# Performance work log

Measured on AMD Instinct MI355X. Metric: run time of the kernel, lower is better.

The kernel has to match this reference:

```python
import jax, jax.numpy as jnp
import numpy as np

HEADS = 16
DIM_HEAD = 64
SCALE = float(np.sqrt(DIM_HEAD))  # NOTE: original code MULTIPLIES by sqrt(dim_head)


def setup_inputs() -> dict:
    key = jax.random.key(0)
    k1, k2, k3, k4 = jax.random.split(key, 4)
    dim = 1024
    b, n = 2, 2048
    s = 1.0 / np.sqrt(dim)
    return {
        "x": jax.random.normal(k1, (b, n, dim), dtype=jnp.float32),
        "w_q": jax.random.normal(k2, (dim, HEADS * DIM_HEAD), dtype=jnp.float32) * s,
        "w_vk": jax.random.normal(k3, (dim, HEADS * DIM_HEAD * 2), dtype=jnp.float32) * s,
        "w_out": jax.random.normal(k4, (HEADS * DIM_HEAD, dim), dtype=jnp.float32) * s,
    }


def reference(x, w_q, w_vk, w_out):
    b, n, _ = x.shape
    h, d = HEADS, DIM_HEAD
    context = x  # context=None, kv_include_self=False
    q = (x @ w_q).reshape(b, n, h, d).transpose(0, 2, 1, 3)          # b h n d
    kv = context @ w_vk                                              # b n 2hd
    k, v = jnp.split(kv, 2, axis=-1)                                 # chunk order: k first, v second
    k = k.reshape(b, n, h, d).transpose(0, 2, 1, 3)
    v = v.reshape(b, n, h, d).transpose(0, 2, 1, 3)
    dots = jnp.einsum('bhid,bhjd->bhij', q, k) * SCALE               # faithful: multiply by sqrt(d)
    attn = jax.nn.softmax(dots, axis=-1)                             # dropout p=0 -> identity
    out = jnp.einsum('bhij,bhjd->bhid', attn, v)
    out = out.transpose(0, 2, 1, 3).reshape(b, n, h * d)
    return out @ w_out
```

## Files before the change

kernel.cpp:

```cpp
#include <hip/hip_runtime.h>

typedef _Float16 half4 __attribute__((ext_vector_type(4)));
typedef _Float16 half8 __attribute__((ext_vector_type(8)));
typedef _Float16 h2pk __attribute__((ext_vector_type(2)));
typedef float f32x4 __attribute__((ext_vector_type(4)));

#define MFMA_F16K32(a, b, c) __builtin_amdgcn_mfma_f32_16x16x32_f16(a, b, c, 0, 0, 0)
#define MFMA_F16K16(a, b, c) __builtin_amdgcn_mfma_f32_16x16x16f16(a, b, c, 0, 0, 0)
#define EXP2F(x) __builtin_amdgcn_exp2f(x)
#define CVT_PK(a, b) __builtin_bit_cast(h2pk, __builtin_amdgcn_cvt_pkrtz(a, b))

constexpr int NSEQ = 2048, DIM = 1024;
constexpr float QSCALE = 11.5415603271f;

__device__ __forceinline__ void ld_lds16(void* lds, const void* g) {
  __builtin_amdgcn_global_load_lds(
      (const __attribute__((address_space(1))) void*)g,
      (__attribute__((address_space(3))) void*)lds, 16, 0, 0);
}

__global__ __launch_bounds__(256) void prep(
    const float* __restrict__ w_q, const float* __restrict__ w_vk,
    const float* __restrict__ w_out, const float* __restrict__ x,
    _Float16* __restrict__ WT, _Float16* __restrict__ WoT,
    _Float16* __restrict__ xf) {
  const int bid = blockIdx.x;
  const int t = threadIdx.x;
  if (bid >= 1024) {
    const size_t i = ((size_t)(bid - 1024) * 256 + t) * 8;
    float4 a = *(const float4*)(x + i), b2 = *(const float4*)(x + i + 4);
    float v[8] = {a.x, a.y, a.z, a.w, b2.x, b2.y, b2.z, b2.w};
    half8 h;
#pragma unroll
    for (int j = 0; j < 8; ++j) h[j] = (_Float16)v[j];
    *(half8*)(xf + i) = h;
    return;
  }
  __shared__ float T[64][65];
  const int bx = bid & 63, k0 = (bid >> 6) * 64;
  const float* src;
  int srcN, n0, dstrow, mode;
  float scale;
  if (bx < 16) {
    src = w_q; srcN = 1024; n0 = bx * 64; dstrow = n0; scale = QSCALE; mode = 0;
  } else if (bx < 48) {
    src = w_vk; srcN = 2048; n0 = (bx - 16) * 64; dstrow = 1024 + n0;
    scale = 1.0f; mode = 0;
  } else {
    src = w_out; srcN = 1024; n0 = (bx - 48) * 64; dstrow = n0;
    scale = 1.0f; mode = 1;
  }
  {
    const int r = t >> 2, c4 = (t & 3) * 16;
    const float* s = src + (size_t)(k0 + r) * srcN + n0 + c4;
    float4 v0 = ((const float4*)s)[0], v1 = ((const float4*)s)[1],
           v2 = ((const float4*)s)[2], v3 = ((const float4*)s)[3];
    *(float4*)&T[r][c4 + 0] = v0;  *(float4*)&T[r][c4 + 4] = v1;
    *(float4*)&T[r][c4 + 8] = v2;  *(float4*)&T[r][c4 + 12] = v3;
  }
  __syncthreads();
  const int rn = t >> 2, kc = (t & 3) * 16;
  half8 hv[2];
#pragma unroll
  for (int half = 0; half < 2; ++half)
#pragma unroll
    for (int j = 0; j < 8; ++j)
      hv[half][j] = (_Float16)(T[kc + half * 8 + j][rn] * scale);
  _Float16* d = ((mode == 0) ? WT + (size_t)(dstrow + rn) * 1024
                             : WoT + (size_t)(n0 + rn) * 1024) + k0 + kc;
  *(half8*)d = hv[0]; *(half8*)(d + 8) = hv[1];
}

__global__ __launch_bounds__(256, 3) void proj6(
    const _Float16* __restrict__ xf, const _Float16* __restrict__ WT,
    _Float16* __restrict__ qb, _Float16* __restrict__ kb,
    _Float16* __restrict__ VT) {
  __shared__ __align__(16) char smem[32768];
  const int t = threadIdx.x;
  const int lane = t & 63, wave = t >> 6, quad = lane >> 4, lq = lane & 15;
  const int bn = blockIdx.x * 128, bm = blockIdx.y * 128;
  const int kind = bn >> 10;
  const int wm = (wave >> 1) * 64, wn = (wave & 1) * 64;

  const int srow = lane >> 2;
  const int schk = (lane & 3) ^ (srow & 3);
  const _Float16* xg = xf + (size_t)(bm + wave * 32 + srow) * DIM + schk * 8;
  const _Float16* bg = WT + (size_t)(bn + wave * 32 + srow) * DIM + schk * 8;
  const int wb = wave * 2048;

  auto issue = [&](char* buf, int k0) {
    ld_lds16(buf + wb,                xg + k0);
    ld_lds16(buf + wb + 1024,         xg + k0 + 16 * DIM);
    ld_lds16(buf + 8192 + wb,         bg + k0);
    ld_lds16(buf + 8192 + wb + 1024,  bg + k0 + 16 * DIM);
  };

  const int swz = (quad ^ (lq & 3)) * 8;

  f32x4 acc[4][4];
#pragma unroll
  for (int i = 0; i < 4; ++i)
#pragma unroll
    for (int j = 0; j < 4; ++j) acc[i][j] = (f32x4){0.f, 0.f, 0.f, 0.f};

  char* bufA = smem;
  char* bufB = smem + 16384;
  issue(bufA, 0);
  for (int k0 = 0; k0 < DIM; k0 += 32) {
    char* cur = ((k0 >> 5) & 1) ? bufB : bufA;
    char* nxt = ((k0 >> 5) & 1) ? bufA : bufB;
    __syncthreads();
    if (k0 + 32 < DIM) issue(nxt, k0 + 32);
    const _Float16* Xs = (const _Float16*)cur;
    const _Float16* Bs = (const _Float16*)(cur + 8192);
    half8 ah[4];
#pragma unroll
    for (int i = 0; i < 4; ++i)
      ah[i] = *(const half8*)&Xs[(wm + i * 16 + lq) * 32 + swz];
#pragma unroll
    for (int j = 0; j < 4; ++j) {
      half8 bf = *(const half8*)&Bs[(wn + j * 16 + lq) * 32 + swz];
#pragma unroll
      for (int i = 0; i < 4; ++i) acc[i][j] = MFMA_F16K32(ah[i], bf, acc[i][j]);
    }
  }

  if (kind == 2) {
#pragma unroll
    for (int i = 0; i < 4; ++i)
#pragma unroll
      for (int j = 0; j < 4; ++j) {
        const int c = (bn - 2048) + wn + j * 16 + lq;
        const int row0 = bm + wm + i * 16 + quad * 4;
        const int b = row0 >> 11, n = row0 & 2047;
        const int h = c >> 6, d = c & 63;
        half4 o;
#pragma unroll
        for (int r = 0; r < 4; ++r) o[r] = (_Float16)acc[i][j][r];
        *(half4*)(VT + ((size_t)(b * 16 + h) * 64 + d) * 2048 + n) = o;
      }
  } else {
    _Float16* D = (kind == 0) ? qb : kb;
    const int cb = bn & 1023;
#pragma unroll
    for (int i = 0; i < 4; ++i)
#pragma unroll
      for (int j = 0; j < 4; ++j) {
        const int col = cb + wn + j * 16 + lq;
#pragma unroll
        for (int r = 0; r < 4; ++r) {
          const int row = bm + wm + i * 16 + quad * 4 + r;
          D[(size_t)row * 1024 + col] = (_Float16)acc[i][j][r];
        }
      }
  }
}

__global__ __launch_bounds__(512, 4) void attn8(
    const _Float16* __restrict__ qb, const _Float16* __restrict__ kb,
    const _Float16* __restrict__ vT, _Float16* __restrict__ ho) {
  __shared__ __align__(16) char smem[65536];
  const int t = threadIdx.x;
  const int lane = t & 63, wave = t >> 6, quad = lane >> 4, lq = lane & 15;
  const int group = wave >> 2, wq = wave & 3;
  const int i0 = blockIdx.x * 128;
  const int bh = blockIdx.y, b = bh >> 4, head = bh & 15;
  const size_t rowbase = (size_t)b * NSEQ;

  half8 qf[2][2];
#pragma unroll
  for (int qt = 0; qt < 2; ++qt) {
    const _Float16* qp =
        qb + (rowbase + i0 + wq * 32 + qt * 16 + lq) * DIM + head * 64 + quad * 8;
    qf[qt][0] = *(const half8*)qp;
    qf[qt][1] = *(const half8*)(qp + 32);
  }

  f32x4 o[2][4];
#pragma unroll
  for (int qt = 0; qt < 2; ++qt)
#pragma unroll
    for (int dt = 0; dt < 4; ++dt) o[qt][dt] = (f32x4){0.f, 0.f, 0.f, 0.f};
  float mrun[2] = {-3.0e38f, -3.0e38f};
  float lrun[2] = {0.f, 0.f};

  const int srow = lane >> 3, schk = (lane & 7) ^ srow;
  const _Float16* kgp =
      kb + (rowbase + wq * 16 + srow) * DIM + head * 64 + schk * 8;
  const _Float16* vgp =
      vT + ((size_t)bh * 64 + wq * 16 + srow) * 2048 + schk * 8;

  auto issue = [&](int bsel, int j) {
    char* kd = smem + (group * 2 + bsel) * 8192 + wq * 2048;
    char* vd = kd + 32768;
    ld_lds16(kd,        kgp + (size_t)j * DIM);
    ld_lds16(kd + 1024, kgp + (size_t)(j + 8) * DIM);
    ld_lds16(vd,        vgp + j);
    ld_lds16(vd + 1024, vgp + 8 * 2048 + j);
  };

  const int swzK0 = (quad ^ (lq & 7)) * 8;
  const int swzK1 = ((quad + 4) ^ (lq & 7)) * 8;

  issue(0, group * 64);

  for (int p = 0; p < 16; ++p) {
    const int cur = p & 1;
    __syncthreads();
    if (p < 15) issue(cur ^ 1, (2 * p + group) * 64 + 128);
    const _Float16* Khs = (const _Float16*)(smem + (group * 2 + cur) * 8192);
    const _Float16* Vts = (const _Float16*)(smem + 32768 + (group * 2 + cur) * 8192);

    f32x4 s[2][4];
    __builtin_amdgcn_s_setprio(1);
#pragma unroll
    for (int nt = 0; nt < 4; ++nt) {
      const int roff = (nt * 16 + lq) * 64;
      half8 k0f = *(const half8*)&Khs[roff + swzK0];
      half8 k1f = *(const half8*)&Khs[roff + swzK1];
#pragma unroll
      for (int qt = 0; qt < 2; ++qt) {
        f32x4 sv = (f32x4){0.f, 0.f, 0.f, 0.f};
        sv = MFMA_F16K32(k0f, qf[qt][0], sv);
        sv = MFMA_F16K32(k1f, qf[qt][1], sv);
        s[qt][nt] = sv;
      }
    }
    __builtin_amdgcn_s_setprio(0);

    half4 pbv[2][4];
#pragma unroll
    for (int qt = 0; qt < 2; ++qt) {
      float m0 = fmaxf(fmaxf(s[qt][0][0], s[qt][0][1]),
                       fmaxf(s[qt][0][2], s[qt][0][3]));
      float m1 = fmaxf(fmaxf(s[qt][1][0], s[qt][1][1]),
                       fmaxf(s[qt][1][2], s[qt][1][3]));
      float m2 = fmaxf(fmaxf(s[qt][2][0], s[qt][2][1]),
                       fmaxf(s[qt][2][2], s[qt][2][3]));
      float m3 = fmaxf(fmaxf(s[qt][3][0], s[qt][3][1]),
                       fmaxf(s[qt][3][2], s[qt][3][3]));
      float mx = fmaxf(fmaxf(m0, m1), fmaxf(m2, m3));
      mx = fmaxf(mx, __shfl_xor(mx, 16));
      mx = fmaxf(mx, __shfl_xor(mx, 32));
      const float mn = fmaxf(mrun[qt], mx);
      const float alpha = EXP2F(mrun[qt] - mn);
      mrun[qt] = mn;
      float rs = 0.f;
#pragma unroll
      for (int nt = 0; nt < 4; ++nt) {
        float p0 = EXP2F(s[qt][nt][0] - mn), p1 = EXP2F(s[qt][nt][1] - mn);
        float p2 = EXP2F(s[qt][nt][2] - mn), p3 = EXP2F(s[qt][nt][3] - mn);
        rs += (p0 + p1) + (p2 + p3);
        h2pk lo = CVT_PK(p0, p1);
        h2pk hi = CVT_PK(p2, p3);
        pbv[qt][nt] = (half4){lo[0], lo[1], hi[0], hi[1]};
      }
      rs += __shfl_xor(rs, 16);
      rs += __shfl_xor(rs, 32);
      lrun[qt] = lrun[qt] * alpha + rs;
#pragma unroll
      for (int dt = 0; dt < 4; ++dt) o[qt][dt] *= alpha;
    }

    __builtin_amdgcn_s_setprio(1);
#pragma unroll
    for (int dt = 0; dt < 4; ++dt) {
      const int vrow = (dt * 16 + lq) * 64;
#pragma unroll
      for (int ntj = 0; ntj < 4; ++ntj) {
        const int voff =
            vrow + (((2 * ntj + (quad >> 1)) ^ (lq & 7)) * 8) + (quad & 1) * 4;
        half4 va = *(const half4*)&Vts[voff];
        o[0][dt] = MFMA_F16K16(va, pbv[0][ntj], o[0][dt]);
        o[1][dt] = MFMA_F16K16(va, pbv[1][ntj], o[1][dt]);
      }
    }
    __builtin_amdgcn_s_setprio(0);
  }

  float* dump = (float*)smem;
  __syncthreads();
  if (group == 1) {
    float* D = dump + wq * 2304 + lane * 36;
#pragma unroll
    for (int qt = 0; qt < 2; ++qt)
#pragma unroll
      for (int dt = 0; dt < 4; ++dt)
        *(f32x4*)(D + (qt * 4 + dt) * 4) = o[qt][dt];
    D[32] = mrun[0]; D[33] = lrun[0]; D[34] = mrun[1]; D[35] = lrun[1];
  }
  __syncthreads();
  _Float16* Ots = (_Float16*)(smem + 40960);
  if (group == 0) {
    const float* D = dump + wq * 2304 + lane * 36;
#pragma unroll
    for (int qt = 0; qt < 2; ++qt) {
      const float m2 = D[32 + qt * 2], l2 = D[33 + qt * 2];
      const float mM = fmaxf(mrun[qt], m2);
      const float f1 = EXP2F(mrun[qt] - mM);
      const float f2 = EXP2F(m2 - mM);
      const float inv = 1.0f / (lrun[qt] * f1 + l2 * f2);
#pragma unroll
      for (int dt = 0; dt < 4; ++dt) {
        f32x4 o2 = *(const f32x4*)(D + (qt * 4 + dt) * 4);
#pragma unroll
        for (int r = 0; r < 4; ++r) {
          const float val = (o[qt][dt][r] * f1 + o2[r] * f2) * inv;
          Ots[(wq * 32 + qt * 16 + lq) * 80 + dt * 16 + quad * 4 + r] =
              (_Float16)val;
        }
      }
    }
  }
  __syncthreads();
  {
    const int row = t >> 2, seg = t & 3;
    const _Float16* src = &Ots[row * 80 + seg * 16];
    half8 o0 = ((const half8*)src)[0], o1 = ((const half8*)src)[1];
    _Float16* dst = ho + (rowbase + i0 + row) * DIM + head * 64 + seg * 16;
    ((half8*)dst)[0] = o0; ((half8*)dst)[1] = o1;
  }
}

__global__ __launch_bounds__(256, 4) void gemm_out(
    const _Float16* __restrict__ A, const _Float16* __restrict__ BT,
    float* __restrict__ C) {
  __shared__ __align__(16) char smem[24576];
  const int t = threadIdx.x;
  const int lane = t & 63, wave = t >> 6, quad = lane >> 4, lq = lane & 15;
  const int bn = blockIdx.x * 128, bm = blockIdx.y * 64;
  const int wm = (wave >> 1) * 32, wn = (wave & 1) * 64;

  const int bco = (lane & 7) ^ (lane >> 3);
  const int brow = 2 * (lane >> 3) + (bco >> 2);
  const int bcc = bco & 3;
  const _Float16* ag = A + (size_t)(bm + wave * 16 + brow) * DIM + bcc * 8;
  const _Float16* bg = BT + (size_t)(bn + wave * 32 + brow) * DIM + bcc * 8;
  const int swzB = ((((lq & 1) << 2) | quad) ^ ((lq >> 1) & 7)) * 8;

  auto issue = [&](char* buf, int k0) {
    ld_lds16(buf + wave * 1024,               ag + k0);
    ld_lds16(buf + 4096 + wave * 2048,        bg + k0);
    ld_lds16(buf + 4096 + wave * 2048 + 1024, bg + k0 + 16 * DIM);
  };

  f32x4 acc[2][4];
#pragma unroll
  for (int i = 0; i < 2; ++i)
#pragma unroll
    for (int j = 0; j < 4; ++j) acc[i][j] = (f32x4){0.f, 0.f, 0.f, 0.f};

  char* bufA = smem;
  char* bufB = smem + 12288;
  issue(bufA, 0);
  for (int k0 = 0; k0 < DIM; k0 += 32) {
    char* cur = ((k0 >> 5) & 1) ? bufB : bufA;
    char* nxt = ((k0 >> 5) & 1) ? bufA : bufB;
    __syncthreads();
    if (k0 + 32 < DIM) issue(nxt, k0 + 32);
    const _Float16* Ahs = (const _Float16*)cur;
    const _Float16* Bhs = (const _Float16*)(cur + 4096);
    half8 ah[2];
#pragma unroll
    for (int i = 0; i < 2; ++i) {
      const int row = wm + i * 16 + lq;
      ah[i] = *(const half8*)&Ahs[(row >> 1) * 64 + swzB];
    }
#pragma unroll
    for (int j = 0; j < 4; ++j) {
      const int row = wn + j * 16 + lq;
      half8 bf = *(const half8*)&Bhs[(row >> 1) * 64 + swzB];
#pragma unroll
      for (int i = 0; i < 2; ++i) acc[i][j] = MFMA_F16K32(ah[i], bf, acc[i][j]);
    }
  }
#pragma unroll
  for (int i = 0; i < 2; ++i)
#pragma unroll
    for (int j = 0; j < 4; ++j) {
      const int col = bn + wn + j * 16 + lq;
#pragma unroll
      for (int r = 0; r < 4; ++r) {
        const int row = bm + wm + i * 16 + quad * 4 + r;
        C[(size_t)row * 1024 + col] = acc[i][j][r];
      }
    }
}

extern "C" void kernel_launch(void* const* d_in, const int* in_sizes, int n_in,
                              void* d_out, int out_size, void* d_ws,
                              size_t ws_size, hipStream_t stream) {
  const float* x     = (const float*)d_in[0];
  const float* w_q   = (const float*)d_in[1];
  const float* w_vk  = (const float*)d_in[2];
  const float* w_out = (const float*)d_in[3];
  float* out = (float*)d_out;

  char* w = (char*)d_ws;
  _Float16* wT  = (_Float16*)(w);
  _Float16* woT = (_Float16*)(w + (6ull << 20));
  _Float16* qbb = (_Float16*)(w + (8ull << 20));
  _Float16* kbb = (_Float16*)(w + (16ull << 20));
  _Float16* vTb = (_Float16*)(w + (24ull << 20));
  _Float16* hob = (_Float16*)(w + (32ull << 20));
  _Float16* xfb = (_Float16*)(w + (40ull << 20));

  dim3 blk(256);
  prep<<<dim3(3072), blk, 0, stream>>>(w_q, w_vk, w_out, x, wT, woT, xfb);
  proj6<<<dim3(24, 32), blk, 0, stream>>>(xfb, wT, qbb, kbb, vTb);
  attn8<<<dim3(16, 32), dim3(512), 0, stream>>>(qbb, kbb, vTb, hob);
  gemm_out<<<dim3(8, 64), blk, 0, stream>>>(hob, woT, out);
}
```

Measured before the change: 189.1 us.

## Stage V-transpose stores through LDS, remap attention blocks per XCD, raise proj occupancy

The V-projection epilogue now writes tiles into LDS and then emits contiguous 64-byte rows of the transposed V buffer, replacing scattered 8-byte stores. The attention kernel remaps block IDs so that all query tiles of one batch-head land on the same XCD, improving L2 reuse of K/V. proj6's launch bounds are raised to 4 blocks per CU. The trade-offs are extra barriers and LDS round-trips in the epilogue, and possible register spills from the tighter occupancy bound.

Result: no change. 186.0 us (-1.6%).

```diff
diff --git a/kernel.cpp b/kernel.cpp
--- a/kernel.cpp
+++ b/kernel.cpp
@@ -62,16 +62,16 @@
   const int rn = t >> 2, kc = (t & 3) * 16;
   half8 hv[2];
 #pragma unroll
-  for (int half = 0; half < 2; ++half)
+  for (int hh = 0; hh < 2; ++hh)
 #pragma unroll
     for (int j = 0; j < 8; ++j)
-      hv[half][j] = (_Float16)(T[kc + half * 8 + j][rn] * scale);
+      hv[hh][j] = (_Float16)(T[kc + hh * 8 + j][rn] * scale);
   _Float16* d = ((mode == 0) ? WT + (size_t)(dstrow + rn) * 1024
                              : WoT + (size_t)(n0 + rn) * 1024) + k0 + kc;
   *(half8*)d = hv[0]; *(half8*)(d + 8) = hv[1];
 }
 
-__global__ __launch_bounds__(256, 3) void proj6(
+__global__ __launch_bounds__(256, 4) void proj6(
     const _Float16* __restrict__ xf, const _Float16* __restrict__ WT,
     _Float16* __restrict__ qb, _Float16* __restrict__ kb,
     _Float16* __restrict__ VT) {
@@ -126,19 +126,40 @@
   }
 
   if (kind == 2) {
-#pragma unroll
-    for (int i = 0; i < 4; ++i)
-#pragma unroll
-      for (int j = 0; j < 4; ++j) {
-        const int c = (bn - 2048) + wn + j * 16 + lq;
-        const int row0 = bm + wm + i * 16 + quad * 4;
-        const int b = row0 >> 11, n = row0 & 2047;
-        const int h = c >> 6, d = c & 63;
-        half4 o;
-#pragma unroll
-        for (int r = 0; r < 4; ++r) o[r] = (_Float16)acc[i][j][r];
-        *(half4*)(VT + ((size_t)(b * 16 + h) * 64 + d) * 2048 + n) = o;
-      }
+    _Float16* Ols = (_Float16*)smem;
+    const int cb = bn - 2048;
+    __syncthreads();
+#pragma unroll
+    for (int pass = 0; pass < 2; ++pass) {
+      if ((wave >> 1) == pass) {
+#pragma unroll
+        for (int i = 0; i < 4; ++i)
+#pragma unroll
+          for (int j = 0; j < 4; ++j) {
+            const int c = wn + j * 16 + lq;
+            const int tl = i * 16 + quad * 4;
+            half4 o;
+#pragma unroll
+            for (int r = 0; r < 4; ++r) o[r] = (_Float16)acc[i][j][r];
+            *(half4*)&Ols[c * 68 + tl] = o;
+          }
+      }
+      __syncthreads();
+      {
+        const int c = t >> 1, hf = t & 1;
+        const int gcol = cb + c;
+        const int tok0 = bm + pass * 64 + hf * 32;
+        const int b2 = tok0 >> 11, n2 = tok0 & 2047;
+        const _Float16* src = &Ols[c * 68 + hf * 32];
+        half8 v0 = ((const half8*)src)[0], v1 = ((const half8*)src)[1],
+              v2 = ((const half8*)src)[2], v3 = ((const half8*)src)[3];
+        _Float16* dst =
+            VT + ((size_t)(b2 * 16 + (gcol >> 6)) * 64 + (gcol & 63)) * 2048 + n2;
+        ((half8*)dst)[0] = v0; ((half8*)dst)[1] = v1;
+        ((half8*)dst)[2] = v2; ((half8*)dst)[3] = v3;
+      }
+      __syncthreads();
+    }
   } else {
     _Float16* D = (kind == 0) ? qb : kb;
     const int cb = bn & 1023;
@@ -163,8 +184,11 @@
   const int t = threadIdx.x;
   const int lane = t & 63, wave = t >> 6, quad = lane >> 4, lq = lane & 15;
   const int group = wave >> 2, wq = wave & 3;
-  const int i0 = blockIdx.x * 128;
-  const int bh = blockIdx.y, b = bh >> 4, head = bh & 15;
+  const int wid = blockIdx.x + 16 * blockIdx.y;
+  const int xcd = wid & 7, slot = wid >> 3;
+  const int i0 = (slot & 15) * 128;
+  const int bh = xcd + 8 * (slot >> 4);
+  const int b = bh >> 4, head = bh & 15;
   const size_t rowbase = (size_t)b * NSEQ;
 
   half8 qf[2][2];
```
